# Performance work log

Hardware: AMD Instinct MI355X
Metric: run time of the kernel (lower is better)

Reference implementation:

```python
import jax, jax.numpy as jnp
import numpy as np

D_MODEL = 768
NUM_HEADS = 48
HEAD_CH = D_MODEL // NUM_HEADS  # 16
INNER = 3 * D_MODEL
BATCH = 2
SEQLEN = 2048
SKIP = 1.0
EPS = 1e-6


def setup_inputs() -> dict:
    key = jax.random.key(0)
    ks = jax.random.split(key, 9)
    s_in = 1.0 / np.sqrt(D_MODEL)
    s_out = 1.0 / np.sqrt(D_MODEL)
    return {
        "inputs": jax.random.normal(ks[0], (BATCH, SEQLEN, D_MODEL), jnp.float32),
        "w_in": jax.random.normal(ks[1], (INNER, D_MODEL), jnp.float32) * s_in,
        "b_in": jax.random.normal(ks[2], (INNER,), jnp.float32) * 0.01,
        "w_sf": jax.random.normal(ks[3], (INNER, 3), jnp.float32) * 0.3,  # depthwise conv kernel
        "b_sf": jax.random.normal(ks[4], (INNER,), jnp.float32) * 0.01,
        "h": jax.random.normal(ks[5], (NUM_HEADS, SEQLEN), jnp.float32) * 0.02,  # long filter
        "norm_w": jnp.ones((D_MODEL,), jnp.float32),
        "w_out": jax.random.normal(ks[6], (D_MODEL, D_MODEL), jnp.float32) * s_out,
        "b_out": jax.random.normal(ks[7], (D_MODEL,), jnp.float32) * 0.01,
    }


def reference(inputs, w_in, b_in, w_sf, b_sf, h, norm_w, w_out, b_out):
    B, L, D = inputs.shape
    N, HC = NUM_HEADS, HEAD_CH
    # in_proj: [B, L, 3D]
    u = jnp.einsum('bld,ed->ble', inputs, w_in) + b_in
    u = jnp.transpose(u, (0, 2, 1))  # [B, 3D, L]
    # causal depthwise conv1d, kernel 3, left pad 2
    up = jnp.pad(u, ((0, 0), (0, 0), (2, 0)))
    uc = (w_sf[:, 0:1] * up[:, :, 0:L]
          + w_sf[:, 1:2] * up[:, :, 1:L + 1]
          + w_sf[:, 2:3] * up[:, :, 2:L + 2]
          + b_sf[:, None])  # [B, 3D, L]
    uc = uc.reshape(B, N, 3 * HC, L)
    x0 = uc[:, :, 0:HC, :]            # q  [B, N, HC, L]
    x1 = uc[:, :, HC:2 * HC, :]       # k  [B, N, HC, L]
    v = uc[:, :, 2 * HC:3 * HC, :]    # v  [B, N, HC, L]
    # outer product: [B, HC_i, HC_j, N, L]
    kv = jnp.einsum('bnil,bnjl->bijnl', x1, v)
    # FFT long convolution with h [N, L], broadcast over b,i,j
    fft_size = 2 * L
    k_f = jnp.fft.rfft(h, n=fft_size) / fft_size        # [N, L+1]
    u_f = jnp.fft.rfft(kv, n=fft_size, axis=-1)         # [B, HC, HC, N, L+1]
    hkv = jnp.fft.irfft(u_f * k_f, n=fft_size, axis=-1, norm='forward')[..., :L]
    # contract with q: [B, L, N, HC_j]
    qhkv = jnp.einsum('bijnl,bnil->blnj', hkv, x0)
    y = qhkv.reshape(B, L, D)
    # RMSNorm
    ms = jnp.mean(jnp.square(y), axis=-1, keepdims=True)
    y = y * jax.lax.rsqrt(ms + EPS) * norm_w
    # out_proj + skip
    y = jnp.einsum('bld,ed->ble', y, w_out) + b_out
    return y + inputs * SKIP
```

## Files before the change

### kernel.cpp

```cpp
#include <hip/hip_runtime.h>
#include <hip/hip_bf16.h>
#include <stdint.h>

typedef __bf16 bf16;
typedef __bf16 bf16x4 __attribute__((ext_vector_type(4)));
typedef __bf16 bf16x8 __attribute__((ext_vector_type(8)));
typedef float f32x4 __attribute__((ext_vector_type(4)));
typedef float f32x16 __attribute__((ext_vector_type(16)));

#define D_MODEL 768
#define NUM_HEADS 48
#define HEAD_CH 16
#define INNER 2304
#define BATCH 2
#define SEQLEN 2048
#define M_ROWS (BATCH * SEQLEN)
#define EPSF 1e-6f

__device__ inline void gload_lds16(const void* g, void* l) {
  __builtin_amdgcn_global_load_lds((__attribute__((address_space(1))) void*)(g),
                                   (__attribute__((address_space(3))) void*)(l),
                                   16, 0, 0);
}

__global__ __launch_bounds__(256) void cvt2_f32_bf16(
    const float* __restrict__ a, bf16* __restrict__ da, int na4,
    const float* __restrict__ b, bf16* __restrict__ db, int nb4) {
  int j = blockIdx.x * 256 + threadIdx.x;
  const float* s;
  bf16* d;
  if (j < na4) {
    s = a; d = da;
  } else {
    j -= na4;
    if (j >= nb4) return;
    s = b; d = db;
  }
  const float4 v = ((const float4*)s)[j];
  bf16x4 o;
  o[0] = (bf16)v.x; o[1] = (bf16)v.y; o[2] = (bf16)v.z; o[3] = (bf16)v.w;
  ((bf16x4*)d)[j] = o;
}

__global__ __launch_bounds__(256) void cvt_f32_bf16(
    const float* __restrict__ src, bf16* __restrict__ dst, int n4) {
  const int i = blockIdx.x * 256 + threadIdx.x;
  if (i < n4) {
    const float4 v = ((const float4*)src)[i];
    bf16x4 o;
    o[0] = (bf16)v.x; o[1] = (bf16)v.y; o[2] = (bf16)v.z; o[3] = (bf16)v.w;
    ((bf16x4*)dst)[i] = o;
  }
}

template <int TM, int TN, int NCOLS, bool ADD_SKIP, typename CT>
__global__ __launch_bounds__(256) void gemm_bt(
    const bf16* __restrict__ A, const bf16* __restrict__ W,
    const float* __restrict__ bias, const float* __restrict__ skip,
    CT* __restrict__ C, int K) {
  constexpr int MI = TM / 32;
  constexpr int NI = TN / 32;
  __shared__ __align__(16) bf16 As[TM * 32];
  __shared__ __align__(16) bf16 Bs[TN * 32];
  const int t = threadIdx.x;
  const int lane = t & 63, w = t >> 6;
  const int wm = (w >> 1) * (TM / 2), wn = (w & 1) * (TN / 2);
  const int row16 = lane & 15, quad = lane >> 4;
  const int m0 = blockIdx.x * TM, n0 = blockIdx.y * TN;

  f32x4 zero4 = {0.f, 0.f, 0.f, 0.f};
  f32x4 acc[MI][NI];
#pragma unroll
  for (int mi = 0; mi < MI; ++mi)
#pragma unroll
    for (int ni = 0; ni < NI; ++ni) acc[mi][ni] = zero4;

  const int arow = t >> 2;
  const int acol = (t & 3) * 8;
  const bf16* Ab = A + (size_t)m0 * K;
  const bf16* Wb = W + (size_t)n0 * K;

  for (int kt = 0; kt < K; kt += 32) {
    gload_lds16(Ab + (size_t)arow * K + kt + acol, As + t * 8);
    if (TM == 128)
      gload_lds16(Ab + (size_t)(64 + arow) * K + kt + acol, As + 2048 + t * 8);
    gload_lds16(Wb + (size_t)arow * K + kt + acol, Bs + t * 8);
    if (TN == 128)
      gload_lds16(Wb + (size_t)(64 + arow) * K + kt + acol, Bs + 2048 + t * 8);
    __syncthreads();

    bf16x8 af[MI], wf[NI];
#pragma unroll
    for (int mi = 0; mi < MI; ++mi)
      af[mi] = *(const bf16x8*)&As[(wm + mi * 16 + row16) * 32 + quad * 8];
#pragma unroll
    for (int ni = 0; ni < NI; ++ni)
      wf[ni] = *(const bf16x8*)&Bs[(wn + ni * 16 + row16) * 32 + quad * 8];
#pragma unroll
    for (int mi = 0; mi < MI; ++mi)
#pragma unroll
      for (int ni = 0; ni < NI; ++ni)
        acc[mi][ni] = __builtin_amdgcn_mfma_f32_16x16x32_bf16(
            af[mi], wf[ni], acc[mi][ni], 0, 0, 0);
    __syncthreads();
  }

#pragma unroll
  for (int mi = 0; mi < MI; ++mi) {
#pragma unroll
    for (int ni = 0; ni < NI; ++ni) {
      const int col = n0 + wn + ni * 16 + row16;
      const float bv = bias[col];
#pragma unroll
      for (int r = 0; r < 4; ++r) {
        const int row = m0 + wm + mi * 16 + quad * 4 + r;
        float v = acc[mi][ni][r] + bv;
        if (ADD_SKIP) v += skip[(size_t)row * NCOLS + col];
        C[(size_t)row * NCOLS + col] = (CT)v;
      }
    }
  }
}

__global__ __launch_bounds__(256) void conv_qkv(
    const bf16* __restrict__ u, const float* __restrict__ w_sf,
    const float* __restrict__ b_sf, bf16* __restrict__ qq,
    bf16* __restrict__ kk, bf16* __restrict__ vv) {
  const int nh = blockIdx.x, b = blockIdx.y, lc = blockIdx.z;
  const int l0 = lc * 128;
  __shared__ __align__(8) bf16 ut[130 * 48];
  const int t = threadIdx.x;
  for (int i = t; i < 130 * 12; i += 256) {
    const int lr = i / 12, qd = i % 12;
    const int l = l0 - 2 + lr;
    uint2 val;
    val.x = 0u; val.y = 0u;
    if (l >= 0)
      val = *(const uint2*)&u[(size_t)(b * SEQLEN + l) * INNER + nh * 48 + qd * 4];
    *(uint2*)&ut[lr * 48 + qd * 4] = val;
  }
  __syncthreads();
  const size_t bn = (size_t)(b * NUM_HEADS + nh);
#pragma unroll
  for (int s = 0; s < 2; ++s) {
    bf16* dst = (s == 0) ? qq : kk;
    const int cb = s * 16;
    for (int i = t; i < 128 * 16; i += 256) {
      const int c = i & 15, lr = i >> 4;
      const int e = nh * 48 + cb + c;
      const float val = w_sf[e * 3 + 0] * (float)ut[lr * 48 + cb + c] +
                        w_sf[e * 3 + 1] * (float)ut[(lr + 1) * 48 + cb + c] +
                        w_sf[e * 3 + 2] * (float)ut[(lr + 2) * 48 + cb + c] +
                        b_sf[e];
      dst[(bn * SEQLEN + l0 + lr) * 16 + c] = (bf16)val;
    }
  }
  for (int i = t; i < 128 * 16; i += 256) {
    const int lr = i & 127, c = i >> 7;
    const int e = nh * 48 + 32 + c;
    const float val = w_sf[e * 3 + 0] * (float)ut[lr * 48 + 32 + c] +
                      w_sf[e * 3 + 1] * (float)ut[(lr + 1) * 48 + 32 + c] +
                      w_sf[e * 3 + 2] * (float)ut[(lr + 2) * 48 + 32 + c] +
                      b_sf[e];
    vv[(bn * 16 + c) * SEQLEN + l0 + lr] = (bf16)val;
  }
}

__global__ __launch_bounds__(256) void attn_kernel(
    const bf16* __restrict__ qq, const bf16* __restrict__ kk,
    const bf16* __restrict__ vv, const float* __restrict__ hg,
    float* __restrict__ y) {
  const int nh = blockIdx.x, b = blockIdx.y;
  const int q32 = (int)gridDim.z - 1 - (int)blockIdx.z;
  const int l0 = q32 * 32;
  __shared__ __align__(16) float hs[32 + SEQLEN];
  __shared__ __align__(16) bf16 st[4 * 32 * 40];
  const int t = threadIdx.x;
  const int n4 = (l0 + 64) >> 2;
  for (int i = t; i < n4; i += 256) {
    float4 val = {0.f, 0.f, 0.f, 0.f};
    if (i >= 8) val = ((const float4*)(hg + nh * SEQLEN))[i - 8];
    ((float4*)hs)[i] = val;
  }
  __syncthreads();

  const int w = t >> 6, lane = t & 63;
  const int l31 = lane & 31, hi = lane >> 5;
  const int row16 = lane & 15, quad = lane >> 4;
  const size_t bn = (size_t)(b * NUM_HEADS + nh);
  const bf16* qb = qq + bn * SEQLEN * 16;
  const bf16* kb = kk + bn * SEQLEN * 16;
  const bf16* vb = vv + bn * 16 * SEQLEN;

  bf16x8 zf;
#pragma unroll
  for (int j = 0; j < 8; ++j) zf[j] = (bf16)0.f;
  const f32x4 zacc4 = {0.f, 0.f, 0.f, 0.f};
  f32x16 zacc16;
#pragma unroll
  for (int j = 0; j < 16; ++j) zacc16[j] = 0.f;

  const bf16x8 qf = *(const bf16x8*)&qb[(l0 + l31) * 16 + hi * 8];

  f32x4 o0 = zacc4, o1 = zacc4;
  bf16* sw = &st[w * 32 * 40];

  int mc = w * 32;
  bf16x8 kf = zf, vf = zf;
  if (mc <= l0) {
    kf = *(const bf16x8*)&kb[(mc + l31) * 16 + hi * 8];
    vf = *(const bf16x8*)&vb[row16 * SEQLEN + mc + quad * 8];
  }
  for (; mc <= l0; mc += 128) {
    const int mn = mc + 128;
    bf16x8 kf2 = zf, vf2 = zf;
    if (mn <= l0) {
      kf2 = *(const bf16x8*)&kb[(mn + l31) * 16 + hi * 8];
      vf2 = *(const bf16x8*)&vb[row16 * SEQLEN + mn + quad * 8];
    }
    f32x16 s = __builtin_amdgcn_mfma_f32_32x32x16_bf16(kf, qf, zacc16, 0, 0, 0);

    const int d0 = 32 + (l0 - mc) + l31 - 4 * hi;
#pragma unroll
    for (int g = 0; g < 4; ++g) {
      const float* hp = &hs[d0 - 8 * g - 3];
      bf16x4 pk;
      pk[0] = (bf16)(s[4 * g + 0] * hp[3]);
      pk[1] = (bf16)(s[4 * g + 1] * hp[2]);
      pk[2] = (bf16)(s[4 * g + 2] * hp[1]);
      pk[3] = (bf16)(s[4 * g + 3] * hp[0]);
      *(bf16x4*)&sw[l31 * 40 + 8 * g + 4 * hi] = pk;
    }
    asm volatile("s_waitcnt lgkmcnt(0)" ::: "memory");
    const bf16x8 sf0 = *(const bf16x8*)&sw[row16 * 40 + quad * 8];
    const bf16x8 sf1 = *(const bf16x8*)&sw[(row16 + 16) * 40 + quad * 8];
    o0 = __builtin_amdgcn_mfma_f32_16x16x32_bf16(sf0, vf, o0, 0, 0, 0);
    o1 = __builtin_amdgcn_mfma_f32_16x16x32_bf16(sf1, vf, o1, 0, 0, 0);
    asm volatile("" ::: "memory");
    kf = kf2; vf = vf2;
  }

  float* ob = (float*)&st[w * 32 * 40];
#pragma unroll
  for (int r = 0; r < 4; ++r) {
    ob[(quad * 4 + r) * 16 + row16] = o0[r];
    ob[(quad * 4 + r + 16) * 16 + row16] = o1[r];
  }
  __syncthreads();
  for (int i = t; i < 32 * 16; i += 256) {
    const int l = i >> 4, j = i & 15;
    float sum = 0.f;
#pragma unroll
    for (int ww = 0; ww < 4; ++ww)
      sum += ((const float*)&st[ww * 32 * 40])[l * 16 + j];
    y[((size_t)(b * SEQLEN + l0 + l) * NUM_HEADS + nh) * 16 + j] = sum;
  }
}

__global__ __launch_bounds__(256) void rmsnorm_k(
    const float* __restrict__ y, const float* __restrict__ nw,
    bf16* __restrict__ yn) {
  const int row = blockIdx.x;
  const int t = threadIdx.x;
  const float* yr = y + (size_t)row * D_MODEL;
  const float v0 = yr[t];
  const float v1 = yr[t + 256];
  const float v2 = yr[t + 512];
  float ss = v0 * v0 + v1 * v1 + v2 * v2;
#pragma unroll
  for (int off = 32; off >= 1; off >>= 1) ss += __shfl_down(ss, off, 64);
  __shared__ float red[4];
  if ((t & 63) == 0) red[t >> 6] = ss;
  __syncthreads();
  const float tot = red[0] + red[1] + red[2] + red[3];
  const float r = rsqrtf(tot * (1.f / 768.f) + EPSF);
  bf16* yo = yn + (size_t)row * D_MODEL;
  yo[t] = (bf16)(v0 * r * nw[t]);
  yo[t + 256] = (bf16)(v1 * r * nw[t + 256]);
  yo[t + 512] = (bf16)(v2 * r * nw[t + 512]);
}

extern "C" void kernel_launch(void* const* d_in, const int* in_sizes, int n_in,
                              void* d_out, int out_size, void* d_ws,
                              size_t ws_size, hipStream_t stream) {
  const float* inputs = (const float*)d_in[0];
  const float* w_in = (const float*)d_in[1];
  const float* b_in = (const float*)d_in[2];
  const float* w_sf = (const float*)d_in[3];
  const float* b_sf = (const float*)d_in[4];
  const float* hb = (const float*)d_in[5];
  const float* norm_w = (const float*)d_in[6];
  const float* w_out = (const float*)d_in[7];
  const float* b_out = (const float*)d_in[8];

  char* ws = (char*)d_ws;
  const size_t U_B = (size_t)M_ROWS * INNER * 2;
  const size_t V_B = (size_t)BATCH * NUM_HEADS * HEAD_CH * SEQLEN * 2;
  const size_t SLOT_B = (size_t)M_ROWS * D_MODEL * 2;
  bf16* u = (bf16*)(ws);
  bf16* wout16 = (bf16*)(ws);
  bf16* yn = (bf16*)(ws + (2 << 20));
  bf16* v = (bf16*)(ws + U_B);
  bf16* in16 = (bf16*)(ws + U_B + V_B);
  bf16* k16 = in16;
  bf16* win16 = (bf16*)(ws + U_B + V_B + SLOT_B);
  bf16* q16 = win16;
  float* y = (float*)d_out;
  float* out = (float*)d_out;

  const int n4_in = M_ROWS * D_MODEL / 4;
  const int n4_win = INNER * D_MODEL / 4;
  const int n4_wout = D_MODEL * D_MODEL / 4;
  hipLaunchKernelGGL(cvt2_f32_bf16, dim3((n4_in + n4_win + 255) / 256),
                     dim3(256), 0, stream, inputs, in16, n4_in, w_in, win16,
                     n4_win);

  hipLaunchKernelGGL((gemm_bt<128, 128, INNER, false, bf16>), dim3(32, 18),
                     dim3(256), 0, stream, in16, win16, b_in,
                     (const float*)nullptr, u, 768);
  hipLaunchKernelGGL(conv_qkv, dim3(48, 2, 16), dim3(256), 0, stream, u, w_sf,
                     b_sf, q16, k16, v);
  hipLaunchKernelGGL(cvt_f32_bf16, dim3((n4_wout + 255) / 256), dim3(256), 0,
                     stream, w_out, wout16, n4_wout);
  hipLaunchKernelGGL(attn_kernel, dim3(48, 2, 64), dim3(256), 0, stream, q16,
                     k16, v, hb, y);
  hipLaunchKernelGGL(rmsnorm_k, dim3(M_ROWS), dim3(256), 0, stream, y, norm_w,
                     yn);
  hipLaunchKernelGGL((gemm_bt<64, 64, D_MODEL, true, float>), dim3(64, 12),
                     dim3(256), 0, stream, yn, wout16, b_out, inputs, out,
                     768);
}
```

Baseline: 190.4 us.

## Store attention output in bf16, shrink LDS stride, retile input GEMM

```diff
diff --git a/kernel.cpp b/kernel.cpp
--- a/kernel.cpp
+++ b/kernel.cpp
@@ -16,6 +16,7 @@
 #define SEQLEN 2048
 #define M_ROWS (BATCH * SEQLEN)
 #define EPSF 1e-6f
+#define SST 36
 
 __device__ inline void gload_lds16(const void* g, void* l) {
   __builtin_amdgcn_global_load_lds((__attribute__((address_space(1))) void*)(g),
@@ -169,12 +170,12 @@
 __global__ __launch_bounds__(256) void attn_kernel(
     const bf16* __restrict__ qq, const bf16* __restrict__ kk,
     const bf16* __restrict__ vv, const float* __restrict__ hg,
-    float* __restrict__ y) {
+    bf16* __restrict__ y) {
   const int nh = blockIdx.x, b = blockIdx.y;
   const int q32 = (int)gridDim.z - 1 - (int)blockIdx.z;
   const int l0 = q32 * 32;
   __shared__ __align__(16) float hs[32 + SEQLEN];
-  __shared__ __align__(16) bf16 st[4 * 32 * 40];
+  __shared__ __align__(16) bf16 st[4 * 32 * SST];
   const int t = threadIdx.x;
   const int n4 = (l0 + 64) >> 2;
   for (int i = t; i < n4; i += 256) {
@@ -203,7 +204,7 @@
   const bf16x8 qf = *(const bf16x8*)&qb[(l0 + l31) * 16 + hi * 8];
 
   f32x4 o0 = zacc4, o1 = zacc4;
-  bf16* sw = &st[w * 32 * 40];
+  bf16* sw = &st[w * 32 * SST];
 
   int mc = w * 32;
   bf16x8 kf = zf, vf = zf;
@@ -229,18 +230,18 @@
       pk[1] = (bf16)(s[4 * g + 1] * hp[2]);
       pk[2] = (bf16)(s[4 * g + 2] * hp[1]);
       pk[3] = (bf16)(s[4 * g + 3] * hp[0]);
-      *(bf16x4*)&sw[l31 * 40 + 8 * g + 4 * hi] = pk;
+      *(bf16x4*)&sw[l31 * SST + 8 * g + 4 * hi] = pk;
     }
     asm volatile("s_waitcnt lgkmcnt(0)" ::: "memory");
-    const bf16x8 sf0 = *(const bf16x8*)&sw[row16 * 40 + quad * 8];
-    const bf16x8 sf1 = *(const bf16x8*)&sw[(row16 + 16) * 40 + quad * 8];
+    const bf16x8 sf0 = *(const bf16x8*)&sw[row16 * SST + quad * 8];
+    const bf16x8 sf1 = *(const bf16x8*)&sw[(row16 + 16) * SST + quad * 8];
     o0 = __builtin_amdgcn_mfma_f32_16x16x32_bf16(sf0, vf, o0, 0, 0, 0);
     o1 = __builtin_amdgcn_mfma_f32_16x16x32_bf16(sf1, vf, o1, 0, 0, 0);
     asm volatile("" ::: "memory");
     kf = kf2; vf = vf2;
   }
 
-  float* ob = (float*)&st[w * 32 * 40];
+  float* ob = (float*)&st[w * 32 * SST];
 #pragma unroll
   for (int r = 0; r < 4; ++r) {
     ob[(quad * 4 + r) * 16 + row16] = o0[r];
@@ -252,20 +253,20 @@
     float sum = 0.f;
 #pragma unroll
     for (int ww = 0; ww < 4; ++ww)
-      sum += ((const float*)&st[ww * 32 * 40])[l * 16 + j];
-    y[((size_t)(b * SEQLEN + l0 + l) * NUM_HEADS + nh) * 16 + j] = sum;
+      sum += ((const float*)&st[ww * 32 * SST])[l * 16 + j];
+    y[((size_t)(b * SEQLEN + l0 + l) * NUM_HEADS + nh) * 16 + j] = (bf16)sum;
   }
 }
 
 __global__ __launch_bounds__(256) void rmsnorm_k(
-    const float* __restrict__ y, const float* __restrict__ nw,
+    const bf16* __restrict__ y, const float* __restrict__ nw,
     bf16* __restrict__ yn) {
   const int row = blockIdx.x;
   const int t = threadIdx.x;
-  const float* yr = y + (size_t)row * D_MODEL;
-  const float v0 = yr[t];
-  const float v1 = yr[t + 256];
-  const float v2 = yr[t + 512];
+  const bf16* yr = y + (size_t)row * D_MODEL;
+  const float v0 = (float)yr[t];
+  const float v1 = (float)yr[t + 256];
+  const float v2 = (float)yr[t + 512];
   float ss = v0 * v0 + v1 * v1 + v2 * v2;
 #pragma unroll
   for (int off = 32; off >= 1; off >>= 1) ss += __shfl_down(ss, off, 64);
@@ -300,12 +301,12 @@
   bf16* u = (bf16*)(ws);
   bf16* wout16 = (bf16*)(ws);
   bf16* yn = (bf16*)(ws + (2 << 20));
+  bf16* y16 = (bf16*)(ws + (9 << 20));
   bf16* v = (bf16*)(ws + U_B);
   bf16* in16 = (bf16*)(ws + U_B + V_B);
   bf16* k16 = in16;
   bf16* win16 = (bf16*)(ws + U_B + V_B + SLOT_B);
   bf16* q16 = win16;
-  float* y = (float*)d_out;
   float* out = (float*)d_out;
 
   const int n4_in = M_ROWS * D_MODEL / 4;
@@ -315,7 +316,7 @@
                      dim3(256), 0, stream, inputs, in16, n4_in, w_in, win16,
                      n4_win);
 
-  hipLaunchKernelGGL((gemm_bt<128, 128, INNER, false, bf16>), dim3(32, 18),
+  hipLaunchKernelGGL((gemm_bt<64, 128, INNER, false, bf16>), dim3(64, 18),
                      dim3(256), 0, stream, in16, win16, b_in,
                      (const float*)nullptr, u, 768);
   hipLaunchKernelGGL(conv_qkv, dim3(48, 2, 16), dim3(256), 0, stream, u, w_sf,
@@ -323,9 +324,9 @@
   hipLaunchKernelGGL(cvt_f32_bf16, dim3((n4_wout + 255) / 256), dim3(256), 0,
                      stream, w_out, wout16, n4_wout);
   hipLaunchKernelGGL(attn_kernel, dim3(48, 2, 64), dim3(256), 0, stream, q16,
-                     k16, v, hb, y);
-  hipLaunchKernelGGL(rmsnorm_k, dim3(M_ROWS), dim3(256), 0, stream, y, norm_w,
-                     yn);
+                     k16, v, hb, y16);
+  hipLaunchKernelGGL(rmsnorm_k, dim3(M_ROWS), dim3(256), 0, stream, y16,
+                     norm_w, yn);
   hipLaunchKernelGGL((gemm_bt<64, 64, D_MODEL, true, float>), dim3(64, 12),
                      dim3(256), 0, stream, yn, wout16, b_out, inputs, out,
                      768);
```

Result: slower. 216.6 us (+13.7%).
